# Performance work log

Measured on AMD Instinct MI355X. Metric: run time of the kernel, lower is better.

The kernel has to match this reference:

```python
import jax, jax.numpy as jnp
import numpy as np

B, D, L = 4096, 128, 4
ALPHA = 1.0
SLOPE = 0.1  # LeakyReLU negative slope


def _leaky(h):
    return jnp.where(h > 0, h, SLOPE * h)


def _dleaky(h):
    return jnp.where(h > 0, 1.0, SLOPE).astype(h.dtype)


def setup_inputs() -> dict:
    key = jax.random.key(0)
    ks = jax.random.split(key, 7)
    scale = 0.5 / np.sqrt(D)  # keep residual roughly Lipschitz < 1
    x = jax.random.normal(ks[0], (B, D), jnp.float32)
    W1 = jax.random.normal(ks[1], (L, D, D), jnp.float32) * scale
    b1 = jax.random.normal(ks[2], (L, D), jnp.float32) * 0.01
    W2 = jax.random.normal(ks[3], (L, D, D), jnp.float32) * scale
    b2 = jax.random.normal(ks[4], (L, D), jnp.float32) * 0.01
    W3 = jax.random.normal(ks[5], (L, D, D), jnp.float32) * scale
    b3 = jax.random.normal(ks[6], (L, D), jnp.float32) * 0.01
    return {"x": x, "W1": W1, "b1": b1, "W2": W2, "b2": b2, "W3": W3, "b3": b3}


def reference(x, W1, b1, W2, b2, W3, b3):
    logdet = jnp.zeros(x.shape[0], x.dtype)
    for i in range(L):  # small fixed number of structurally distinct blocks
        w1, w2, w3 = W1[i], W2[i], W3[i]
        # --- block forward: x <- x + alpha * f(x) ---
        h1 = x @ w1.T + b1[i]
        h2 = _leaky(h1) @ w2.T + b2[i]
        f = _leaky(h2) @ w3.T + b3[i]
        x = x + ALPHA * f
        # --- log|det J_f| evaluated at the NEW x (as in the original code) ---
        g1 = x @ w1.T + b1[i]          # [B, D] pre-activation 1
        d1 = _dleaky(g1)
        g2 = _leaky(g1) @ w2.T + b2[i]  # [B, D] pre-activation 2
        d2 = _dleaky(g2)
        # J[b] = w3 @ diag(d2[b]) @ w2 @ diag(d1[b]) @ w1  -> [B, D, D]
        J = (w3[None, :, :] * d2[:, None, :]) @ w2
        J = (J * d1[:, None, :]) @ w1
        s = jnp.linalg.svd(J, compute_uv=False)  # [B, D] singular values
        logdet = logdet + jnp.sum(jnp.log(s), axis=-1)
    return x, logdet
```

## Files before the change

### kernel.cpp

```cpp
#include <hip/hip_runtime.h>

typedef __attribute__((ext_vector_type(8))) short short8;
typedef __attribute__((ext_vector_type(4))) float float4f;
typedef __attribute__((ext_vector_type(4))) unsigned short us4;

#define PITCH 136
#define ROWS 32
#define LOG_SLOPE -2.302585092994046f
#define LN2 0.6931471805599453f
#define NBLK 140
#define LDS_BYTES 69760
#define WS_BIAS 4160
#define WS_WPLANES 8192
#define NWELEM 196608

__device__ __forceinline__ float bf2f(unsigned int u) {
    return __builtin_bit_cast(float, u << 16);
}
__device__ __forceinline__ unsigned short f2bf(float f) {
    unsigned int x = __builtin_bit_cast(unsigned int, f);
    x += 0x7fff + ((x >> 16) & 1);
    return (unsigned short)(x >> 16);
}
__device__ __forceinline__ float4f vmsub(float4f a, float s, float4f b) {
    a[0] -= s * b[0]; a[1] -= s * b[1]; a[2] -= s * b[2]; a[3] -= s * b[3];
    return a;
}
__device__ __forceinline__ float4f vscale(float4f a, float s) {
    a[0] *= s; a[1] *= s; a[2] *= s; a[3] *= s;
    return a;
}

__device__ __forceinline__ void bar_lgkm() {
    asm volatile("s_waitcnt lgkmcnt(0)\n\ts_barrier" ::: "memory");
}

template<int ISF32>
__device__ __forceinline__ float ldv(const void* p, int i) {
    if (ISF32) return ((const float*)p)[i];
    return bf2f(((const unsigned short*)p)[i]);
}

__device__ __forceinline__ int detect_f32(const unsigned short* W1u, int lane) {
    unsigned int u = W1u[lane * 2];
    unsigned int e = (u >> 7) & 0xFF;
    int bad = (e < 64) || (e > 135);
    return __ballot(bad) != 0ull;
}

__device__ __forceinline__ float4f mfma16(short8 a, short8 b, float4f c) {
    return __builtin_amdgcn_mfma_f32_16x16x32_bf16(a, b, c, 0, 0, 0);
}

__device__ __forceinline__ void split8(float4f a, float4f b, short8& hi, short8& lo) {
#pragma unroll
    for (int j = 0; j < 4; ++j) {
        float v = a[j]; unsigned short h = f2bf(v);
        hi[j] = (short)h; lo[j] = (short)f2bf(v - bf2f(h));
        v = b[j]; h = f2bf(v);
        hi[4 + j] = (short)h; lo[4 + j] = (short)f2bf(v - bf2f(h));
    }
}

__global__ void k_prep(const void* __restrict__ W1, const void* __restrict__ W2,
                       const void* __restrict__ W3, const void* __restrict__ b1,
                       const void* __restrict__ b2, const void* __restrict__ b3,
                       float* __restrict__ ws) {
    const int tid = threadIdx.x, bid = blockIdx.x;
    const int isf32 = detect_f32((const unsigned short*)W1, tid & 63);
    unsigned short* whi = (unsigned short*)(ws + WS_WPLANES);
    unsigned short* wlo = whi + NWELEM;
    if (bid < 96) {
        int s = (bid * 256 + tid) * 8;
        int mat = s >> 14, off = s & 16383;
        int wsel = mat >> 2;
        const void* Wm = wsel == 0 ? W1 : (wsel == 1 ? W2 : W3);
        int src = (mat & 3) * 16384 + off;
        short8 hi, lo;
        if (isf32) {
            const float* p = (const float*)Wm + src;
            split8(*(const float4f*)p, *(const float4f*)(p + 4), hi, lo);
        } else {
            hi = *(const short8*)((const unsigned short*)Wm + src);
            lo = (short8){0, 0, 0, 0, 0, 0, 0, 0};
        }
        int c = off >> 7, k = off & 127;
        int kk = k >> 5, q = (k >> 3) & 3;
        int cb = c >> 4, m = c & 15;
        int noff = kk * 4096 + cb * 512 + m * 32 + q * 8;
        *(short8*)(whi + mat * 16384 + noff) = hi;
        *(short8*)(wlo + mat * 16384 + noff) = lo;
    } else {
        for (int e = tid; e < 1536; e += 256) {
            int bsel = e >> 9, idx = e & 511;
            const void* bp = bsel == 0 ? b1 : (bsel == 1 ? b2 : b3);
            ws[WS_BIAS + e] = isf32 ? ((const float*)bp)[idx]
                                    : bf2f(((const unsigned short*)bp)[idx]);
        }
        if (tid == 0) ((int*)ws)[0] = 0;
    }
}

struct W8 { short8 v[16]; };

__device__ __forceinline__ W8 loadW(const unsigned short* __restrict__ wh,
                                    const unsigned short* __restrict__ wl,
                                    int cb, int mq) {
    W8 r;
#pragma unroll
    for (int kk = 0; kk < 4; ++kk) {
        const int o0 = kk * 4096 + cb * 512 + mq;
        const int o1 = o0 + 512;
        r.v[kk * 4 + 0] = *(const short8*)(wh + o0);
        r.v[kk * 4 + 1] = *(const short8*)(wh + o1);
        r.v[kk * 4 + 2] = *(const short8*)(wl + o0);
        r.v[kk * 4 + 3] = *(const short8*)(wl + o1);
    }
    return r;
}

template<int MODE, int DOLOAD>
__device__ __forceinline__ W8 matvec(const W8& w,
        const unsigned short* inh, const unsigned short* inl,
        unsigned short* outh, unsigned short* outl,
        const unsigned short* resh, const unsigned short* resl,
        const unsigned short* __restrict__ nwh, const unsigned short* __restrict__ nwl,
        const float* __restrict__ bias,
        int lane, int colb, int* cnt) {
    const int m = lane & 15, q = lane >> 4;
    float4f b0 = *(const float4f*)(bias + colb + q * 4);
    float4f b1 = *(const float4f*)(bias + colb + 16 + q * 4);
    float4f acc[2][2];
    acc[0][0] = b0; acc[0][1] = b1;
    acc[1][0] = b0; acc[1][1] = b1;
    bar_lgkm();
    W8 wn;
    if constexpr (DOLOAD) {
        wn = loadW(nwh, nwl, colb >> 4, m * 32 + q * 8);
    }
#pragma unroll
    for (int kk = 0; kk < 4; ++kk) {
        const int kc = kk * 32 + q * 8;
#pragma unroll
        for (int rt = 0; rt < 2; ++rt) {
            short8 xh = *(const short8*)(inh + (rt * 16 + m) * PITCH + kc);
            short8 xl = *(const short8*)(inl + (rt * 16 + m) * PITCH + kc);
            acc[rt][0] = mfma16(w.v[kk * 4 + 0], xh, acc[rt][0]);
            acc[rt][0] = mfma16(w.v[kk * 4 + 0], xl, acc[rt][0]);
            acc[rt][0] = mfma16(w.v[kk * 4 + 2], xh, acc[rt][0]);
            acc[rt][1] = mfma16(w.v[kk * 4 + 1], xh, acc[rt][1]);
            acc[rt][1] = mfma16(w.v[kk * 4 + 1], xl, acc[rt][1]);
            acc[rt][1] = mfma16(w.v[kk * 4 + 3], xh, acc[rt][1]);
        }
    }
    int cc[2] = {0, 0};
#pragma unroll
    for (int rt = 0; rt < 2; ++rt) {
#pragma unroll
        for (int ct = 0; ct < 2; ++ct) {
            float4f v = acc[rt][ct];
            const int o = (rt * 16 + m) * PITCH + colb + ct * 16 + q * 4;
            if (MODE == 1) {
                us4 rh = *(const us4*)(resh + o);
                us4 rl = *(const us4*)(resl + o);
#pragma unroll
                for (int j = 0; j < 4; ++j) v[j] += bf2f(rh[j]) + bf2f(rl[j]);
            }
            if (MODE >= 2) {
#pragma unroll
                for (int j = 0; j < 4; ++j) cc[rt] += (v[j] <= 0.0f) ? 1 : 0;
            }
            if (MODE == 0 || MODE == 2) {
#pragma unroll
                for (int j = 0; j < 4; ++j) v[j] = v[j] > 0.0f ? v[j] : 0.1f * v[j];
            }
            if (MODE != 3) {
                us4 h, l;
#pragma unroll
                for (int j = 0; j < 4; ++j) {
                    unsigned short hh = f2bf(v[j]);
                    h[j] = hh;
                    l[j] = f2bf(v[j] - bf2f(hh));
                }
                *(us4*)(outh + o) = h;
                *(us4*)(outl + o) = l;
            }
        }
    }
    if (MODE >= 2) {
#pragma unroll
        for (int rt = 0; rt < 2; ++rt) {
            int c = cc[rt];
            c += __shfl_xor(c, 16);
            c += __shfl_xor(c, 32);
            if (q == 0) atomicAdd(&cnt[rt * 16 + m], c);
        }
    }
    if constexpr (DOLOAD) return wn;
    else return w;
}

template<int ISF32>
__device__ __forceinline__ void fwd(int bid, int tid, int lane, char* ldsb,
                                    const void* x, const float* ws, void* out,
                                    float* wsw) {
    unsigned short* P = (unsigned short*)ldsb;
    unsigned short* Ah = P;
    unsigned short* Al = P + 1 * ROWS * PITCH;
    unsigned short* Bh = P + 2 * ROWS * PITCH;
    unsigned short* Bl = P + 3 * ROWS * PITCH;
    unsigned short* Th = P + 4 * ROWS * PITCH;
    unsigned short* Tl = P + 5 * ROWS * PITCH;
    unsigned short* Uh = P + 6 * ROWS * PITCH;
    unsigned short* Ul = P + 7 * ROWS * PITCH;
    int* cnt = (int*)(P + 8 * ROWS * PITCH);
    const unsigned short* whi = (const unsigned short*)(ws + WS_WPLANES);
    const unsigned short* wlo = whi + NWELEM;
    const float* bias = ws + WS_BIAS;
    const int r0 = bid * ROWS;
    const int m = lane & 15, q = lane >> 4;
    const int colb = (tid >> 6) * 32;
    W8 wA = loadW(whi, wlo, colb >> 4, m * 32 + q * 8);
    W8 wB, wC;
    for (int e = tid; e < ROWS * 128; e += 256) {
        int r = e >> 7, c = e & 127;
        float v = ldv<ISF32>(x, (r0 + r) * 128 + c);
        unsigned short h = f2bf(v);
        Ah[r * PITCH + c] = h;
        Al[r * PITCH + c] = f2bf(v - bf2f(h));
    }
    if (tid < ROWS) cnt[tid] = 0;
    unsigned short *curh = Ah, *curl = Al, *othh = Bh, *othl = Bl;
#pragma unroll 1
    for (int layer = 0; layer < 4; ++layer) {
        const unsigned short* w2h = whi + (4 + layer) * 16384;
        const unsigned short* w2l = wlo + (4 + layer) * 16384;
        const unsigned short* w3h = whi + (8 + layer) * 16384;
        const unsigned short* w3l = wlo + (8 + layer) * 16384;
        const unsigned short* n1h = whi + ((layer + 1) & 3) * 16384;
        const unsigned short* n1l = wlo + ((layer + 1) & 3) * 16384;
        const float* b1p = bias + layer * 128;
        const float* b2p = bias + 512 + layer * 128;
        const float* b3p = bias + 1024 + layer * 128;
        wB = matvec<0, 1>(wA, curh, curl, Th, Tl, 0, 0, w2h, w2l, b1p, lane, colb, cnt);
        wC = matvec<0, 1>(wB, Th, Tl, Uh, Ul, 0, 0, w3h, w3l, b2p, lane, colb, cnt);
        matvec<1, 0>(wC, Uh, Ul, othh, othl, curh, curl, 0, 0, b3p, lane, colb, cnt);
        matvec<2, 0>(wA, othh, othl, Th, Tl, 0, 0, 0, 0, b1p, lane, colb, cnt);
        wA = matvec<3, 1>(wB, Th, Tl, Th, Tl, 0, 0, n1h, n1l, b2p, lane, colb, cnt);
        unsigned short* t;
        t = curh; curh = othh; othh = t;
        t = curl; curl = othl; othl = t;
    }
    bar_lgkm();
    for (int e = tid; e < ROWS * 128; e += 256) {
        int r = e >> 7, c = e & 127;
        float v = bf2f(curh[r * PITCH + c]) + bf2f(curl[r * PITCH + c]);
        if (ISF32) ((float*)out)[(r0 + r) * 128 + c] = v;
        else ((unsigned short*)out)[(r0 + r) * 128 + c] = f2bf(v);
    }
    if (tid < ROWS) wsw[64 + r0 + tid] = (float)cnt[tid];
}

template<int ISF32>
__device__ __forceinline__ float lu_logdet(int id, int tid, float* lds,
        const void* W1, const void* W2, const void* W3) {
    const int wsel = id % 3;
    const void* Wm = (wsel == 0 ? W1 : (wsel == 1 ? W2 : W3));
    const int ofs = (id / 3) * 16384;
    const int tx = tid & 31, ty = tid >> 5;
    float* rowbuf = lds;
    float* colbuf = lds + 1024;
    float4f V[16];
#pragma unroll
    for (int m = 0; m < 16; ++m) {
        int base = ofs + (ty + 8 * m) * 128 + 4 * tx;
        if (ISF32) {
            V[m] = *(const float4f*)((const float*)Wm + base);
        } else {
            ushort4 u = *(const ushort4*)((const unsigned short*)Wm + base);
            V[m] = (float4f){bf2f(u.x), bf2f(u.y), bf2f(u.z), bf2f(u.w)};
        }
    }
    if (ty < 4) *(float4f*)&rowbuf[ty * 128 + 4 * tx] = V[0];
    if (tx == 0) {
#pragma unroll
        for (int j = 0; j < 4; ++j) {
#pragma unroll
            for (int mg = 0; mg < 4; ++mg) {
                float4f t = {V[mg * 4 + 0][j], V[mg * 4 + 1][j],
                             V[mg * 4 + 2][j], V[mg * 4 + 3][j]};
                *(float4f*)&colbuf[j * 128 + ty * 16 + mg * 4] = t;
            }
        }
    }
    __syncthreads();
    float logacc = 0.0f;
#pragma unroll 1
    for (int kap = 0; kap < 32; ++kap) {
        const int K = kap * 4;
        const int buf = (kap & 1) * 512;
        float4f D[4], R[4], C[4][4];
#pragma unroll
        for (int j = 0; j < 4; ++j) {
            D[j] = *(const float4f*)&rowbuf[buf + j * 128 + K];
            R[j] = *(const float4f*)&rowbuf[buf + j * 128 + 4 * tx];
#pragma unroll
            for (int mg = 0; mg < 4; ++mg)
                C[j][mg] = *(const float4f*)&colbuf[buf + j * 128 + ty * 16 + mg * 4];
        }
        float p0 = D[0][0], i0 = 1.0f / p0;
        float l10 = D[1][0] * i0, l20 = D[2][0] * i0, l30 = D[3][0] * i0;
        D[1] = vmsub(D[1], l10, D[0]); R[1] = vmsub(R[1], l10, R[0]);
        D[2] = vmsub(D[2], l20, D[0]); R[2] = vmsub(R[2], l20, R[0]);
        D[3] = vmsub(D[3], l30, D[0]); R[3] = vmsub(R[3], l30, R[0]);
        float p1 = D[1][1], i1 = 1.0f / p1;
        float l21 = D[2][1] * i1, l31 = D[3][1] * i1;
        D[2] = vmsub(D[2], l21, D[1]); R[2] = vmsub(R[2], l21, R[1]);
        D[3] = vmsub(D[3], l31, D[1]); R[3] = vmsub(R[3], l31, R[1]);
        float p2 = D[2][2], i2 = 1.0f / p2;
        float l32 = D[3][2] * i2;
        D[3] = vmsub(D[3], l32, D[2]); R[3] = vmsub(R[3], l32, R[2]);
        float p3 = D[3][3], i3 = 1.0f / p3;
        logacc += __log2f(fabsf(p0)) + __log2f(fabsf(p1))
                + __log2f(fabsf(p2)) + __log2f(fabsf(p3));
        float4f X3 = vscale(R[3], i3);
        float4f X2 = vscale(vmsub(R[2], D[2][3], X3), i2);
        float4f X1 = vscale(vmsub(vmsub(R[1], D[1][2], X2), D[1][3], X3), i1);
        float4f X0 = vscale(vmsub(vmsub(vmsub(R[0], D[0][1], X1),
                                        D[0][2], X2), D[0][3], X3), i0);
#pragma unroll
        for (int mg = 0; mg < 4; ++mg) {
#pragma unroll
            for (int e = 0; e < 4; ++e) {
                float4f v = V[mg * 4 + e];
                v = vmsub(v, C[0][mg][e], X0);
                v = vmsub(v, C[1][mg][e], X1);
                v = vmsub(v, C[2][mg][e], X2);
                v = vmsub(v, C[3][mg][e], X3);
                V[mg * 4 + e] = v;
            }
        }
        if (kap < 31) {
            const int nbuf = ((kap + 1) & 1) * 512;
            const int tb = (kap & 1) ? 0 : 4;
            const int mn = (kap + 1) >> 1;
            if (ty >= tb && ty < tb + 4) {
                float4f val;
                switch (mn) {
                case 0:  val = V[0];  break; case 1:  val = V[1];  break;
                case 2:  val = V[2];  break; case 3:  val = V[3];  break;
                case 4:  val = V[4];  break; case 5:  val = V[5];  break;
                case 6:  val = V[6];  break; case 7:  val = V[7];  break;
                case 8:  val = V[8];  break; case 9:  val = V[9];  break;
                case 10: val = V[10]; break; case 11: val = V[11]; break;
                case 12: val = V[12]; break; case 13: val = V[13]; break;
                case 14: val = V[14]; break; default: val = V[15]; break;
                }
                *(float4f*)&rowbuf[nbuf + (ty - tb) * 128 + 4 * tx] = val;
            }
            if (tx == kap + 1) {
#pragma unroll
                for (int j = 0; j < 4; ++j) {
#pragma unroll
                    for (int mg = 0; mg < 4; ++mg) {
                        float4f t = {V[mg * 4 + 0][j], V[mg * 4 + 1][j],
                                     V[mg * 4 + 2][j], V[mg * 4 + 3][j]};
                        *(float4f*)&colbuf[nbuf + j * 128 + ty * 16 + mg * 4] = t;
                    }
                }
            }
        }
        __syncthreads();
    }
    return logacc * LN2;
}

__global__ __launch_bounds__(256, 1) void k_main(
        const void* __restrict__ x,
        const void* __restrict__ W1, const void* __restrict__ b1,
        const void* __restrict__ W2, const void* __restrict__ b2,
        const void* __restrict__ W3, const void* __restrict__ b3,
        void* __restrict__ out, float* __restrict__ ws) {
    extern __shared__ __align__(16) char ldsb[];
    __shared__ int s_last;
    const int tid = threadIdx.x;
    const int lane = tid & 63;
    const int isf32 = detect_f32((const unsigned short*)W1, lane);

    if (blockIdx.x < 12) {
        float ld = isf32 ? lu_logdet<1>(blockIdx.x, tid, (float*)ldsb, W1, W2, W3)
                         : lu_logdet<0>(blockIdx.x, tid, (float*)ldsb, W1, W2, W3);
        if (tid == 0) ws[2 + blockIdx.x] = ld;
    } else {
        const int bid = blockIdx.x - 12;
        if (isf32) fwd<1>(bid, tid, lane, ldsb, x, ws, out, ws);
        else       fwd<0>(bid, tid, lane, ldsb, x, ws, out, ws);
    }

    __threadfence();
    if (tid == 0) s_last = (atomicAdd((int*)ws, 1) == NBLK - 1);
    __syncthreads();
    if (!s_last) return;
    __threadfence();
    float s = 0.0f;
#pragma unroll
    for (int i = 0; i < 12; ++i) s += ws[2 + i];
    for (int b = tid; b < 4096; b += 256) {
        float v = s + LOG_SLOPE * ws[64 + b];
        if (isf32) ((float*)out)[524288 + b] = v;
        else ((unsigned short*)out)[524288 + b] = f2bf(v);
    }
}

extern "C" void kernel_launch(void* const* d_in, const int* in_sizes, int n_in,
                              void* d_out, int out_size, void* d_ws, size_t ws_size,
                              hipStream_t stream) {
    const void* x  = d_in[0];
    const void* W1 = d_in[1];
    const void* b1 = d_in[2];
    const void* W2 = d_in[3];
    const void* b2 = d_in[4];
    const void* W3 = d_in[5];
    const void* b3 = d_in[6];
    float* ws = (float*)d_ws;

    hipLaunchKernelGGL(k_prep, dim3(97), dim3(256), 0, stream,
                       W1, W2, W3, b1, b2, b3, ws);
    hipLaunchKernelGGL(k_main, dim3(NBLK), dim3(256), LDS_BYTES, stream,
                       x, W1, b1, W2, b2, W3, b3, d_out, ws);
}
```

Measured before the change: 119.1 us.

## Halve rows per block to 16 and launch twice as many blocks

Cuts each forward block's batch tile from 32 to 16 rows, which halves LDS use and doubles the forward block count. The matvec is reduced to a single 16-row MFMA tile per wave, and launch bounds now allow two blocks per CU. The aim is to fill more CUs and overlap latency better. In exchange, each block reloads the same weight fragments for half as many rows, and the LU logdet blocks now run with a tighter register budget.

Result: slower. 123.3 us (+3.5%).

```diff
diff --git a/kernel.cpp b/kernel.cpp
--- a/kernel.cpp
+++ b/kernel.cpp
@@ -5,11 +5,11 @@
 typedef __attribute__((ext_vector_type(4))) unsigned short us4;
 
 #define PITCH 136
-#define ROWS 32
+#define ROWS 16
 #define LOG_SLOPE -2.302585092994046f
 #define LN2 0.6931471805599453f
-#define NBLK 140
-#define LDS_BYTES 69760
+#define NBLK 268
+#define LDS_BYTES 34880
 #define WS_BIAS 4160
 #define WS_WPLANES 8192
 #define NWELEM 196608
@@ -128,11 +128,8 @@
         const float* __restrict__ bias,
         int lane, int colb, int* cnt) {
     const int m = lane & 15, q = lane >> 4;
-    float4f b0 = *(const float4f*)(bias + colb + q * 4);
-    float4f b1 = *(const float4f*)(bias + colb + 16 + q * 4);
-    float4f acc[2][2];
-    acc[0][0] = b0; acc[0][1] = b1;
-    acc[1][0] = b0; acc[1][1] = b1;
+    float4f acc0 = *(const float4f*)(bias + colb + q * 4);
+    float4f acc1 = *(const float4f*)(bias + colb + 16 + q * 4);
     bar_lgkm();
     W8 wn;
     if constexpr (DOLOAD) {
@@ -141,60 +138,51 @@
 #pragma unroll
     for (int kk = 0; kk < 4; ++kk) {
         const int kc = kk * 32 + q * 8;
-#pragma unroll
-        for (int rt = 0; rt < 2; ++rt) {
-            short8 xh = *(const short8*)(inh + (rt * 16 + m) * PITCH + kc);
-            short8 xl = *(const short8*)(inl + (rt * 16 + m) * PITCH + kc);
-            acc[rt][0] = mfma16(w.v[kk * 4 + 0], xh, acc[rt][0]);
-            acc[rt][0] = mfma16(w.v[kk * 4 + 0], xl, acc[rt][0]);
-            acc[rt][0] = mfma16(w.v[kk * 4 + 2], xh, acc[rt][0]);
-            acc[rt][1] = mfma16(w.v[kk * 4 + 1], xh, acc[rt][1]);
-            acc[rt][1] = mfma16(w.v[kk * 4 + 1], xl, acc[rt][1]);
-            acc[rt][1] = mfma16(w.v[kk * 4 + 3], xh, acc[rt][1]);
-        }
-    }
-    int cc[2] = {0, 0};
-#pragma unroll
-    for (int rt = 0; rt < 2; ++rt) {
-#pragma unroll
-        for (int ct = 0; ct < 2; ++ct) {
-            float4f v = acc[rt][ct];
-            const int o = (rt * 16 + m) * PITCH + colb + ct * 16 + q * 4;
-            if (MODE == 1) {
-                us4 rh = *(const us4*)(resh + o);
-                us4 rl = *(const us4*)(resl + o);
-#pragma unroll
-                for (int j = 0; j < 4; ++j) v[j] += bf2f(rh[j]) + bf2f(rl[j]);
+        short8 xh = *(const short8*)(inh + m * PITCH + kc);
+        short8 xl = *(const short8*)(inl + m * PITCH + kc);
+        acc0 = mfma16(w.v[kk * 4 + 0], xh, acc0);
+        acc0 = mfma16(w.v[kk * 4 + 0], xl, acc0);
+        acc0 = mfma16(w.v[kk * 4 + 2], xh, acc0);
+        acc1 = mfma16(w.v[kk * 4 + 1], xh, acc1);
+        acc1 = mfma16(w.v[kk * 4 + 1], xl, acc1);
+        acc1 = mfma16(w.v[kk * 4 + 3], xh, acc1);
+    }
+    int cc = 0;
+#pragma unroll
+    for (int ct = 0; ct < 2; ++ct) {
+        float4f v = (ct == 0) ? acc0 : acc1;
+        const int o = m * PITCH + colb + ct * 16 + q * 4;
+        if (MODE == 1) {
+            us4 rh = *(const us4*)(resh + o);
+            us4 rl = *(const us4*)(resl + o);
+#pragma unroll
+            for (int j = 0; j < 4; ++j) v[j] += bf2f(rh[j]) + bf2f(rl[j]);
+        }
+        if (MODE >= 2) {
+#pragma unroll
+            for (int j = 0; j < 4; ++j) cc += (v[j] <= 0.0f) ? 1 : 0;
+        }
+        if (MODE == 0 || MODE == 2) {
+#pragma unroll
+            for (int j = 0; j < 4; ++j) v[j] = v[j] > 0.0f ? v[j] : 0.1f * v[j];
+        }
+        if (MODE != 3) {
+            us4 h, l;
+#pragma unroll
+            for (int j = 0; j < 4; ++j) {
+                unsigned short hh = f2bf(v[j]);
+                h[j] = hh;
+                l[j] = f2bf(v[j] - bf2f(hh));
             }
-            if (MODE >= 2) {
-#pragma unroll
-                for (int j = 0; j < 4; ++j) cc[rt] += (v[j] <= 0.0f) ? 1 : 0;
-            }
-            if (MODE == 0 || MODE == 2) {
-#pragma unroll
-                for (int j = 0; j < 4; ++j) v[j] = v[j] > 0.0f ? v[j] : 0.1f * v[j];
-            }
-            if (MODE != 3) {
-                us4 h, l;
-#pragma unroll
-                for (int j = 0; j < 4; ++j) {
-                    unsigned short hh = f2bf(v[j]);
-                    h[j] = hh;
-                    l[j] = f2bf(v[j] - bf2f(hh));
-                }
-                *(us4*)(outh + o) = h;
-                *(us4*)(outl + o) = l;
-            }
+            *(us4*)(outh + o) = h;
+            *(us4*)(outl + o) = l;
         }
     }
     if (MODE >= 2) {
-#pragma unroll
-        for (int rt = 0; rt < 2; ++rt) {
-            int c = cc[rt];
-            c += __shfl_xor(c, 16);
-            c += __shfl_xor(c, 32);
-            if (q == 0) atomicAdd(&cnt[rt * 16 + m], c);
-        }
+        int c = cc;
+        c += __shfl_xor(c, 16);
+        c += __shfl_xor(c, 32);
+        if (q == 0) atomicAdd(&cnt[m], c);
     }
     if constexpr (DOLOAD) return wn;
     else return w;
@@ -375,7 +363,7 @@
     return logacc * LN2;
 }
 
-__global__ __launch_bounds__(256, 1) void k_main(
+__global__ __launch_bounds__(256, 2) void k_main(
         const void* __restrict__ x,
         const void* __restrict__ W1, const void* __restrict__ b1,
         const void* __restrict__ W2, const void* __restrict__ b2,
```
